# Optimization experiments

Measured on AMD Instinct MI355X. Metric: run time of the kernel, lower is better.

Reference implementation:

```python
import jax, jax.numpy as jnp
import numpy as np

B, T, S, O, D = 1024, 512, 8, 4, 64  # batch, seq_len, sensory_dim, output_dim, hidden d (d=64 from target_params=78980)


def _w(key, shape):
    # random weights scaled ~1/sqrt(fan_in); stored as [in, out] so y = x @ W + b
    return jax.random.normal(key, shape, dtype=jnp.float32) / np.sqrt(shape[0]).astype(np.float32)


def setup_inputs() -> dict:
    key = jax.random.key(0)
    ks = jax.random.split(key, 16)
    z = lambda n: jnp.zeros((n,), jnp.float32)
    return {
        "x": jax.random.normal(ks[0], (B, T, S), dtype=jnp.float32),
        "W_enc_w": _w(ks[1], (S, D)), "W_enc_b": z(D),
        "W_from_W": _w(ks[2], (D, D)), "W_from_I": _w(ks[3], (D, D)), "W_from_A": _w(ks[4], (D, D)),
        "W_gate_w": _w(ks[5], (2 * D, D)), "W_gate_b": z(D),
        "I_z_w": _w(ks[6], (3 * D, D)), "I_z_b": z(D),
        "I_r_w": _w(ks[7], (3 * D, D)), "I_r_b": z(D),
        "I_h_w": _w(ks[8], (3 * D, D)), "I_h_b": z(D),
        "A_from_W": _w(ks[9], (D, D)), "A_from_I": _w(ks[10], (D, D)), "A_from_A": _w(ks[11], (D, D)),
        "A_gate_w": _w(ks[12], (2 * D, D)), "A_gate_b": z(D),
        "phi_w": _w(ks[13], (D, O)), "phi_b": z(O),
    }


def reference(x, W_enc_w, W_enc_b, W_from_W, W_from_I, W_from_A, W_gate_w, W_gate_b,
              I_z_w, I_z_b, I_r_w, I_r_b, I_h_w, I_h_b,
              A_from_W, A_from_I, A_from_A, A_gate_w, A_gate_b, phi_w, phi_b):
    batch = x.shape[0]
    d = W_from_W.shape[0]

    def step(carry, x_t):
        W, I, A = carry  # each [B, d]
        xt = jnp.tanh(x_t @ W_enc_w + W_enc_b)
        W_in = xt + W @ W_from_W + I @ W_from_I + A @ W_from_A
        Wg = jax.nn.sigmoid(jnp.concatenate([I, A], -1) @ W_gate_w + W_gate_b)
        W_new = jnp.tanh(W_in) * Wg
        comb = jnp.concatenate([W_new, I, A], -1)  # [B, 3d]
        z = jax.nn.sigmoid(comb @ I_z_w + I_z_b)
        r = jax.nn.sigmoid(comb @ I_r_w + I_r_b)
        h = jnp.tanh(jnp.concatenate([W_new, r * I, A], -1) @ I_h_w + I_h_b)
        I_new = (1.0 - z) * I + z * h
        A_in = W_new @ A_from_W + I_new @ A_from_I + A @ A_from_A
        Ag = jax.nn.sigmoid(jnp.concatenate([W_new, I_new], -1) @ A_gate_w + A_gate_b)
        A_new = jnp.tanh(A_in) * Ag
        action = A_new @ phi_w + phi_b  # [B, O]
        return (W_new, I_new, A_new), action

    init = tuple(jnp.zeros((batch, d), x.dtype) for _ in range(3))
    _, actions = jax.lax.scan(step, init, jnp.swapaxes(x, 0, 1))  # [T, B, O]
    return jnp.swapaxes(actions, 0, 1)  # [B, T, O]
```

## Files before the change

kernel.cpp:

```cpp
#include <hip/hip_runtime.h>
#include <cstddef>
#include <cstdint>

#define T_LEN 512
#define O_DIM 4

typedef _Float16 f16x8 __attribute__((ext_vector_type(8)));
typedef float    f32x4 __attribute__((ext_vector_type(4)));

#define MFMA(a, b, c) __builtin_amdgcn_mfma_f32_16x16x32_f16((a), (b), (c), 0, 0, 0)

__device__ __forceinline__ float sigm_f(float x) {
    return __builtin_amdgcn_rcpf(1.0f + __builtin_amdgcn_exp2f(x * -1.44269504f));
}
__device__ __forceinline__ float tanh_f(float x) {
    float e = __builtin_amdgcn_exp2f(x * 2.88539008f);
    return __builtin_fmaf(-2.0f, __builtin_amdgcn_rcpf(e + 1.0f), 1.0f);
}

__device__ __forceinline__ f16x8 zf8() {
    f16x8 r;
#pragma unroll
    for (int j = 0; j < 8; ++j) r[j] = (_Float16)0.0f;
    return r;
}

__device__ __forceinline__ f16x8 load_bt(const float* __restrict__ W, int k0, int n) {
    const int lane = threadIdx.x & 63;
    const float* p = W + (size_t)(k0 + ((lane >> 4) << 3)) * 64 + n;
    f16x8 r;
#pragma unroll
    for (int j = 0; j < 8; ++j) r[j] = (_Float16)p[(size_t)j * 64];
    return r;
}

__device__ __forceinline__ f16x8 ld_af(const _Float16* base, int kt) {
    const int lane = threadIdx.x & 63;
    const int m = lane & 15, q = lane >> 4;
    return *(const f16x8*)(base + m * 72 + kt * 32 + q * 8);
}

__global__ __launch_bounds__(256, 1) void ANIMAZeroExact_86887188398421_kernel(
    const float* __restrict__ x,
    const float* __restrict__ Wenc_w, const float* __restrict__ Wenc_b,
    const float* __restrict__ WfW, const float* __restrict__ WfI, const float* __restrict__ WfA,
    const float* __restrict__ Wg_w, const float* __restrict__ Wg_b,
    const float* __restrict__ Iz_w, const float* __restrict__ Iz_b,
    const float* __restrict__ Ir_w, const float* __restrict__ Ir_b,
    const float* __restrict__ Ih_w, const float* __restrict__ Ih_b,
    const float* __restrict__ AfW, const float* __restrict__ AfI, const float* __restrict__ AfA,
    const float* __restrict__ Ag_w, const float* __restrict__ Ag_b,
    const float* __restrict__ phi_w, const float* __restrict__ phi_b,
    float* __restrict__ out)
{
    __shared__ __align__(16) _Float16 Wl[16][72];
    __shared__ __align__(16) _Float16 Il[16][72];
    __shared__ __align__(16) _Float16 Al[16][72];
    __shared__ __align__(16) _Float16 Rl[16][72];
    __shared__ __align__(16) float xtile[4 * 132 + 4];
    __shared__ __align__(16) float actb[4][16][4];

    const int tid  = threadIdx.x;
    const int w    = tid >> 6;
    const int lane = tid & 63;
    const int q    = lane >> 4;
    const int c    = lane & 15;
    const int n    = w * 16 + c;
    const int r0   = blockIdx.x * 4;

    for (int i = tid; i < 16 * 72; i += 256) {
        (&Wl[0][0])[i] = (_Float16)0.0f; (&Il[0][0])[i] = (_Float16)0.0f;
        (&Al[0][0])[i] = (_Float16)0.0f; (&Rl[0][0])[i] = (_Float16)0.0f;
    }

    f16x8 S1B[6], G1B[4], ZB[6], RB[6], HB[6], AB[6], AGB[4], phiB[2];
#pragma unroll
    for (int j = 0; j < 2; ++j) {
        S1B[j] = load_bt(WfW, 32 * j, n);  S1B[2 + j] = load_bt(WfI, 32 * j, n);  S1B[4 + j] = load_bt(WfA, 32 * j, n);
        AB[j]  = load_bt(AfW, 32 * j, n);  AB[2 + j]  = load_bt(AfI, 32 * j, n);  AB[4 + j]  = load_bt(AfA, 32 * j, n);
    }
#pragma unroll
    for (int j = 0; j < 4; ++j) { G1B[j] = load_bt(Wg_w, 32 * j, n); AGB[j] = load_bt(Ag_w, 32 * j, n); }
#pragma unroll
    for (int j = 0; j < 6; ++j) { ZB[j] = load_bt(Iz_w, 32 * j, n); RB[j] = load_bt(Ir_w, 32 * j, n); HB[j] = load_bt(Ih_w, 32 * j, n); }
#pragma unroll
    for (int kt = 0; kt < 2; ++kt)
#pragma unroll
        for (int j = 0; j < 8; ++j) {
            int k = kt * 32 + q * 8 + j;
            phiB[kt][j] = (c < O_DIM) ? (_Float16)phi_w[k * O_DIM + c] : (_Float16)0.0f;
        }

    float We[8];
#pragma unroll
    for (int j = 0; j < 8; ++j) We[j] = Wenc_w[j * 64 + n];

    const float bias_g  = Wg_b[n],  bias_z = Iz_b[n], bias_r = Ir_b[n];
    const float bias_h  = Ih_b[n],  bias_ag = Ag_b[n], bias_e = Wenc_b[n];
    const float bias_p  = (c < O_DIM) ? phi_b[c] : 0.0f;

    f32x4 zero4 = {0.f, 0.f, 0.f, 0.f};

    if (tid < 64) {
        const int row = tid >> 4, su = tid & 15;
        const float* xg = x + (size_t)(r0 + row) * (T_LEN * 8) + (1 + su) * 8;
        float4 a = *(const float4*)(xg);
        float4 b = *(const float4*)(xg + 4);
        float* d = &xtile[row * 132 + su * 8];
        *(float4*)d = a; *(float4*)(d + 4) = b;
    }
    float xt;
    {
        const float* xg = x + (size_t)(r0 + q) * (T_LEN * 8);
        float4 a = *(const float4*)(xg);
        float4 b = *(const float4*)(xg + 4);
        float d = bias_e;
        d = __builtin_fmaf(a.x, We[0], d); d = __builtin_fmaf(a.y, We[1], d);
        d = __builtin_fmaf(a.z, We[2], d); d = __builtin_fmaf(a.w, We[3], d);
        d = __builtin_fmaf(b.x, We[4], d); d = __builtin_fmaf(b.y, We[5], d);
        d = __builtin_fmaf(b.z, We[6], d); d = __builtin_fmaf(b.w, We[7], d);
        xt = tanh_f(d);
    }

    f32x4 w_a = zero4, w_b = zero4, g_a = zero4, g_b = zero4;
    f32x4 zp_a = zero4, zp_c = zero4, rp_a = zero4, rp_c = zero4;
    f32x4 hp_a, hp_c, ap_a, ap_c, ag_a, ag_c;
    float Iv = 0.f;
    f16x8 nW0, nW1;

    __syncthreads();

#pragma unroll 1
    for (int t = 0; t < T_LEN; ++t) {
        const bool fl = ((t & 15) == 0) && (t > 0);
        const int tw = t & 3;

        f16x8 sA0 = ld_af(&Al[0][0], 0), sA1 = ld_af(&Al[0][0], 1);
        float4 xla = {0,0,0,0}, xlb = {0,0,0,0};
        if (fl && tid < 64) {
            const int row = tid >> 4, su = tid & 15;
            int off = (t + 1 + su) * 8;
            if (off > T_LEN * 8 - 8) off = T_LEN * 8 - 8;
            const float* xg = x + (size_t)(r0 + row) * (T_LEN * 8) + off;
            xla = *(const float4*)(xg); xlb = *(const float4*)(xg + 4);
        }
        w_a = MFMA(sA0, S1B[4], w_a);  w_b = MFMA(sA1, S1B[5], w_b);
        g_a = MFMA(sA0, G1B[2], g_a);  g_b = MFMA(sA1, G1B[3], g_b);
        {
            float wn = tanh_f(xt + w_a[0] + w_b[0]) * sigm_f(g_a[0] + g_b[0] + bias_g);
            Wl[4 * q][n] = (_Float16)wn;
        }
        zp_a = MFMA(sA0, ZB[4], zp_a);  zp_c = MFMA(sA1, ZB[5], zp_c);
        rp_a = MFMA(sA0, RB[4], rp_a);  rp_c = MFMA(sA1, RB[5], rp_c);
        __syncthreads();

        nW0 = ld_af(&Wl[0][0], 0); nW1 = ld_af(&Wl[0][0], 1);
        hp_a = MFMA(sA0, HB[4], zero4); hp_c = MFMA(sA1, HB[5], zero4);
        ap_a = MFMA(sA0, AB[4], zero4); ap_c = MFMA(sA1, AB[5], zero4);
        if (w == tw) {
            f32x4 act = MFMA(sA0, phiB[0], zero4);
            act = MFMA(sA1, phiB[1], act);
            if (t > 0 && c < O_DIM)
                actb[q][(t - 1) & 15][c] = act[0] + bias_p;
        }
        rp_a = MFMA(nW0, RB[0], rp_a);  rp_c = MFMA(nW1, RB[1], rp_c);
        {
            float rv = sigm_f(rp_a[0] + rp_c[0] + bias_r);
            Rl[4 * q][n] = (_Float16)(rv * Iv);
        }
        zp_a = MFMA(nW0, ZB[0], zp_a);  zp_c = MFMA(nW1, ZB[1], zp_c);
        hp_a = MFMA(nW0, HB[0], hp_a);  hp_c = MFMA(nW1, HB[1], hp_c);
        w_a  = MFMA(nW0, S1B[0], zero4); w_b = MFMA(nW1, S1B[1], zero4);
        if (fl && tid < 64) {
            const int row = tid >> 4, su = tid & 15;
            float* d = &xtile[row * 132 + su * 8];
            *(float4*)d = xla; *(float4*)(d + 4) = xlb;
        }
        __syncthreads();

        f16x8 hR0 = ld_af(&Rl[0][0], 0), hR1 = ld_af(&Rl[0][0], 1);
        const float* xs = &xtile[q * 132 + (t & 15) * 8];
        float4 qa = *(const float4*)xs;
        float4 qb = *(const float4*)(xs + 4);
        ap_a = MFMA(nW0, AB[0], ap_a);  ap_c = MFMA(nW1, AB[1], ap_c);
        float zv = sigm_f(zp_a[0] + zp_c[0] + bias_z);
        float xtn;
        {
            float d = bias_e;
            d = __builtin_fmaf(qa.x, We[0], d); d = __builtin_fmaf(qa.y, We[1], d);
            d = __builtin_fmaf(qa.z, We[2], d); d = __builtin_fmaf(qa.w, We[3], d);
            d = __builtin_fmaf(qb.x, We[4], d); d = __builtin_fmaf(qb.y, We[5], d);
            d = __builtin_fmaf(qb.z, We[6], d); d = __builtin_fmaf(qb.w, We[7], d);
            xtn = tanh_f(d);
        }
        if (fl && tid < 64) {
            const int row = tid >> 4, sl = tid & 15;
            float4 av = *(const float4*)(&actb[row][sl][0]);
            *(float4*)(out + (size_t)(r0 + row) * (T_LEN * O_DIM) + (t - 16 + sl) * 4) = av;
        }
        hp_a = MFMA(hR0, HB[2], hp_a);  hp_c = MFMA(hR1, HB[3], hp_c);
        {
            float hv = tanh_f(hp_a[0] + hp_c[0] + bias_h);
            Iv = __builtin_fmaf(zv, hv - Iv, Iv);
            Il[4 * q][n] = (_Float16)Iv;
        }
        ag_a = MFMA(nW0, AGB[0], zero4); ag_c = MFMA(nW1, AGB[1], zero4);
        __syncthreads();

        f16x8 nI0 = ld_af(&Il[0][0], 0), nI1 = ld_af(&Il[0][0], 1);
        ap_a = MFMA(nI0, AB[2], ap_a);  ap_c = MFMA(nI1, AB[3], ap_c);
        ag_a = MFMA(nI0, AGB[2], ag_a); ag_c = MFMA(nI1, AGB[3], ag_c);
        {
            float av = tanh_f(ap_a[0] + ap_c[0]) * sigm_f(ag_a[0] + ag_c[0] + bias_ag);
            Al[4 * q][n] = (_Float16)av;
        }
        w_a = MFMA(nI0, S1B[2], w_a);   w_b = MFMA(nI1, S1B[3], w_b);
        g_a = MFMA(nI0, G1B[0], zero4); g_b = MFMA(nI1, G1B[1], zero4);
        zp_a = MFMA(nI0, ZB[2], zero4); zp_c = MFMA(nI1, ZB[3], zero4);
        rp_a = MFMA(nI0, RB[2], zero4); rp_c = MFMA(nI1, RB[3], zero4);
        xt = xtn;
        __syncthreads();
    }

    {
        f16x8 eA0 = ld_af(&Al[0][0], 0), eA1 = ld_af(&Al[0][0], 1);
        if (w == 0) {
            f32x4 act = MFMA(eA0, phiB[0], zero4);
            act = MFMA(eA1, phiB[1], act);
            if (c < O_DIM)
                actb[q][15][c] = act[0] + bias_p;
        }
        __syncthreads();
        if (tid < 64) {
            const int row = tid >> 4, sl = tid & 15;
            float4 av = *(const float4*)(&actb[row][sl][0]);
            *(float4*)(out + (size_t)(r0 + row) * (T_LEN * O_DIM) + (496 + sl) * 4) = av;
        }
    }
}

extern "C" void kernel_launch(void* const* d_in, const int* in_sizes, int n_in,
                              void* d_out, int out_size, void* d_ws, size_t ws_size,
                              hipStream_t stream) {
    ANIMAZeroExact_86887188398421_kernel<<<dim3(256), dim3(256), 0, stream>>>(
        (const float*)d_in[0],
        (const float*)d_in[1],  (const float*)d_in[2],
        (const float*)d_in[3],  (const float*)d_in[4],  (const float*)d_in[5],
        (const float*)d_in[6],  (const float*)d_in[7],
        (const float*)d_in[8],  (const float*)d_in[9],
        (const float*)d_in[10], (const float*)d_in[11],
        (const float*)d_in[12], (const float*)d_in[13],
        (const float*)d_in[14], (const float*)d_in[15], (const float*)d_in[16],
        (const float*)d_in[17], (const float*)d_in[18],
        (const float*)d_in[19], (const float*)d_in[20],
        (float*)d_out);
}
```

Before: 497.8 us.

## Batch phi projection over 16-step A history and widen x/output staging

Each step's A state is now saved into a 16-step history buffer, so the per-step phi MFMA on one wave is replaced by a batched projection every 16 steps that packs timestep×row pairs into full MFMA tiles. The x prefetch and output flush are widened to 64-step chunks handled by all 256 threads, which cuts how often those branches fire inside the serial recurrence. The cost is more shared memory and a heavier burst of work on flush iterations.

```diff
diff --git a/kernel.cpp b/kernel.cpp
--- a/kernel.cpp
+++ b/kernel.cpp
@@ -16,13 +16,6 @@
 __device__ __forceinline__ float tanh_f(float x) {
     float e = __builtin_amdgcn_exp2f(x * 2.88539008f);
     return __builtin_fmaf(-2.0f, __builtin_amdgcn_rcpf(e + 1.0f), 1.0f);
-}
-
-__device__ __forceinline__ f16x8 zf8() {
-    f16x8 r;
-#pragma unroll
-    for (int j = 0; j < 8; ++j) r[j] = (_Float16)0.0f;
-    return r;
 }
 
 __device__ __forceinline__ f16x8 load_bt(const float* __restrict__ W, int k0, int n) {
@@ -57,8 +50,9 @@
     __shared__ __align__(16) _Float16 Il[16][72];
     __shared__ __align__(16) _Float16 Al[16][72];
     __shared__ __align__(16) _Float16 Rl[16][72];
-    __shared__ __align__(16) float xtile[4 * 132 + 4];
-    __shared__ __align__(16) float actb[4][16][4];
+    __shared__ __align__(16) _Float16 Ahist[16][4][72];
+    __shared__ __align__(16) float xbig[4][520];
+    __shared__ __align__(16) float actb[4][64][4];
 
     const int tid  = threadIdx.x;
     const int w    = tid >> 6;
@@ -101,13 +95,13 @@
 
     f32x4 zero4 = {0.f, 0.f, 0.f, 0.f};
 
-    if (tid < 64) {
-        const int row = tid >> 4, su = tid & 15;
-        const float* xg = x + (size_t)(r0 + row) * (T_LEN * 8) + (1 + su) * 8;
-        float4 a = *(const float4*)(xg);
-        float4 b = *(const float4*)(xg + 4);
-        float* d = &xtile[row * 132 + su * 8];
-        *(float4*)d = a; *(float4*)(d + 4) = b;
+    {
+        const int prow = tid >> 6, psu = tid & 63;
+        const float* xg = x + (size_t)(r0 + prow) * (T_LEN * 8) + (1 + psu) * 8;
+        float4 pa = *(const float4*)(xg);
+        float4 pb = *(const float4*)(xg + 4);
+        float* d = &xbig[prow][psu * 8];
+        *(float4*)d = pa; *(float4*)(d + 4) = pb;
     }
     float xt;
     {
@@ -132,17 +126,17 @@
 
 #pragma unroll 1
     for (int t = 0; t < T_LEN; ++t) {
-        const bool fl = ((t & 15) == 0) && (t > 0);
-        const int tw = t & 3;
+        const bool fl16 = ((t & 15) == 0) && (t > 0);
+        const bool fl64 = ((t & 63) == 0) && (t > 0);
 
         f16x8 sA0 = ld_af(&Al[0][0], 0), sA1 = ld_af(&Al[0][0], 1);
-        float4 xla = {0,0,0,0}, xlb = {0,0,0,0};
-        if (fl && tid < 64) {
-            const int row = tid >> 4, su = tid & 15;
-            int off = (t + 1 + su) * 8;
+        float4 xra = {0,0,0,0}, xrb = {0,0,0,0};
+        if (fl64) {
+            const int rrow = tid >> 6, rsu = tid & 63;
+            int off = (t + 1 + rsu) * 8;
             if (off > T_LEN * 8 - 8) off = T_LEN * 8 - 8;
-            const float* xg = x + (size_t)(r0 + row) * (T_LEN * 8) + off;
-            xla = *(const float4*)(xg); xlb = *(const float4*)(xg + 4);
+            const float* xg = x + (size_t)(r0 + rrow) * (T_LEN * 8) + off;
+            xra = *(const float4*)(xg); xrb = *(const float4*)(xg + 4);
         }
         w_a = MFMA(sA0, S1B[4], w_a);  w_b = MFMA(sA1, S1B[5], w_b);
         g_a = MFMA(sA0, G1B[2], g_a);  g_b = MFMA(sA1, G1B[3], g_b);
@@ -157,11 +151,19 @@
         nW0 = ld_af(&Wl[0][0], 0); nW1 = ld_af(&Wl[0][0], 1);
         hp_a = MFMA(sA0, HB[4], zero4); hp_c = MFMA(sA1, HB[5], zero4);
         ap_a = MFMA(sA0, AB[4], zero4); ap_c = MFMA(sA1, AB[5], zero4);
-        if (w == tw) {
-            f32x4 act = MFMA(sA0, phiB[0], zero4);
-            act = MFMA(sA1, phiB[1], act);
-            if (t > 0 && c < O_DIM)
-                actb[q][(t - 1) & 15][c] = act[0] + bias_p;
+        if (fl16) {
+            const _Float16* ah = &Ahist[0][0][0];
+            const int hw = (4 * w + (c >> 2)) * 288 + (c & 3) * 72 + 8 * q;
+            f16x8 a0 = *(const f16x8*)(ah + hw);
+            f16x8 a1 = *(const f16x8*)(ah + hw + 32);
+            f32x4 act = MFMA(a0, phiB[0], zero4);
+            act = MFMA(a1, phiB[1], act);
+            if (c < O_DIM) {
+                const int slot = (t - 16 + 4 * w + q) & 63;
+#pragma unroll
+                for (int rg = 0; rg < 4; ++rg)
+                    actb[rg][slot][c] = act[rg] + bias_p;
+            }
         }
         rp_a = MFMA(nW0, RB[0], rp_a);  rp_c = MFMA(nW1, RB[1], rp_c);
         {
@@ -171,15 +173,15 @@
         zp_a = MFMA(nW0, ZB[0], zp_a);  zp_c = MFMA(nW1, ZB[1], zp_c);
         hp_a = MFMA(nW0, HB[0], hp_a);  hp_c = MFMA(nW1, HB[1], hp_c);
         w_a  = MFMA(nW0, S1B[0], zero4); w_b = MFMA(nW1, S1B[1], zero4);
-        if (fl && tid < 64) {
-            const int row = tid >> 4, su = tid & 15;
-            float* d = &xtile[row * 132 + su * 8];
-            *(float4*)d = xla; *(float4*)(d + 4) = xlb;
+        if (fl64) {
+            const int rrow = tid >> 6, rsu = tid & 63;
+            float* d = &xbig[rrow][rsu * 8];
+            *(float4*)d = xra; *(float4*)(d + 4) = xrb;
         }
         __syncthreads();
 
         f16x8 hR0 = ld_af(&Rl[0][0], 0), hR1 = ld_af(&Rl[0][0], 1);
-        const float* xs = &xtile[q * 132 + (t & 15) * 8];
+        const float* xs = &xbig[q][(t & 63) * 8];
         float4 qa = *(const float4*)xs;
         float4 qb = *(const float4*)(xs + 4);
         ap_a = MFMA(nW0, AB[0], ap_a);  ap_c = MFMA(nW1, AB[1], ap_c);
@@ -193,10 +195,10 @@
             d = __builtin_fmaf(qb.z, We[6], d); d = __builtin_fmaf(qb.w, We[7], d);
             xtn = tanh_f(d);
         }
-        if (fl && tid < 64) {
-            const int row = tid >> 4, sl = tid & 15;
-            float4 av = *(const float4*)(&actb[row][sl][0]);
-            *(float4*)(out + (size_t)(r0 + row) * (T_LEN * O_DIM) + (t - 16 + sl) * 4) = av;
+        if (fl64) {
+            const int frow = tid >> 6, fs = tid & 63;
+            float4 av = *(const float4*)(&actb[frow][fs][0]);
+            *(float4*)(out + (size_t)(r0 + frow) * (T_LEN * O_DIM) + (t - 64 + fs) * 4) = av;
         }
         hp_a = MFMA(hR0, HB[2], hp_a);  hp_c = MFMA(hR1, HB[3], hp_c);
         {
@@ -213,6 +215,7 @@
         {
             float av = tanh_f(ap_a[0] + ap_c[0]) * sigm_f(ag_a[0] + ag_c[0] + bias_ag);
             Al[4 * q][n] = (_Float16)av;
+            Ahist[t & 15][q][n] = (_Float16)av;
         }
         w_a = MFMA(nI0, S1B[2], w_a);   w_b = MFMA(nI1, S1B[3], w_b);
         g_a = MFMA(nI0, G1B[0], zero4); g_b = MFMA(nI1, G1B[1], zero4);
@@ -223,19 +226,22 @@
     }
 
     {
-        f16x8 eA0 = ld_af(&Al[0][0], 0), eA1 = ld_af(&Al[0][0], 1);
-        if (w == 0) {
-            f32x4 act = MFMA(eA0, phiB[0], zero4);
-            act = MFMA(eA1, phiB[1], act);
-            if (c < O_DIM)
-                actb[q][15][c] = act[0] + bias_p;
-        }
-        __syncthreads();
-        if (tid < 64) {
-            const int row = tid >> 4, sl = tid & 15;
-            float4 av = *(const float4*)(&actb[row][sl][0]);
-            *(float4*)(out + (size_t)(r0 + row) * (T_LEN * O_DIM) + (496 + sl) * 4) = av;
-        }
+        const _Float16* ah = &Ahist[0][0][0];
+        const int hw = (4 * w + (c >> 2)) * 288 + (c & 3) * 72 + 8 * q;
+        f16x8 a0 = *(const f16x8*)(ah + hw);
+        f16x8 a1 = *(const f16x8*)(ah + hw + 32);
+        f32x4 act = MFMA(a0, phiB[0], zero4);
+        act = MFMA(a1, phiB[1], act);
+        if (c < O_DIM) {
+            const int slot = 48 + 4 * w + q;
+#pragma unroll
+            for (int rg = 0; rg < 4; ++rg)
+                actb[rg][slot][c] = act[rg] + bias_p;
+        }
+        __syncthreads();
+        const int frow = tid >> 6, fs = tid & 63;
+        float4 av = *(const float4*)(&actb[frow][fs][0]);
+        *(float4*)(out + (size_t)(r0 + frow) * (T_LEN * O_DIM) + (448 + fs) * 4) = av;
     }
 }
 
```

Result: faster. 458.5 us (-7.9%).
